# Performance work log

Measured on AMD Instinct MI355X. Metric: run time of the kernel, lower is better.

Reference implementation:

```python
import jax, jax.numpy as jnp
import numpy as np

N = 50000   # num_nodes
T = 8       # num_time_steps
C = 64      # feature width (num_features == hidden == num_classes == 64, forced by the module's shape constraints)
E = 800000  # num_edges


def temporal_conv(x, edge_index, time_index, W, b, perturb=None):
    """Faithful TemporalAGNNConv.forward: per-timestep masked scatter-add of
    neighbor features, concat over T, linear + relu. Implemented as a single
    fused (t, dst)-bucketed segment reduce instead of T separate propagates.
    Note: self.lin is dead code in the original; self-loop addition in the
    original would crash (time_index length mismatch) so edges are used as-is.
    """
    src, dst = edge_index[0], edge_index[1]
    msgs = x[src]                                   # [E, C] gather
    seg = time_index * N + dst                      # combined (t, node) bucket
    agg = jax.ops.segment_sum(msgs, seg, num_segments=T * N)   # [T*N, C]
    cat = agg.reshape(T, N, C).transpose(1, 0, 2).reshape(N, T * C)  # [N, T*C]
    out = jax.nn.relu(cat @ W + b)                  # temporal_lin + relu
    if perturb is not None:
        out = out + perturb
    return out


def setup_inputs() -> dict:
    key = jax.random.key(0)
    ks = jax.random.split(key, 11)
    x = jax.random.normal(ks[0], (N, C), jnp.float32)
    edge_index = jax.random.randint(ks[1], (2, E), 0, N, dtype=jnp.int32)
    time_index = jax.random.randint(ks[2], (E,), 0, T, dtype=jnp.int32)
    s_t = 1.0 / np.sqrt(T * C).astype(np.float32)
    # temporal_lin weights stored as [in, out] (torch Linear transposed)
    Wt1 = jax.random.uniform(ks[3], (T * C, C), jnp.float32, -s_t, s_t)
    bt1 = jax.random.uniform(ks[4], (C,), jnp.float32, -s_t, s_t)
    Wt2 = jax.random.uniform(ks[5], (T * C, C), jnp.float32, -s_t, s_t)
    bt2 = jax.random.uniform(ks[6], (C,), jnp.float32, -s_t, s_t)
    s_a1 = 1.0 / np.sqrt(C).astype(np.float32)
    Wa1 = jax.random.uniform(ks[7], (C, 128), jnp.float32, -s_a1, s_a1)
    ba1 = jax.random.uniform(ks[8], (128,), jnp.float32, -s_a1, s_a1)
    s_a2 = 1.0 / np.sqrt(128).astype(np.float32)
    Wa2 = jax.random.uniform(ks[9], (128, C), jnp.float32, -s_a2, s_a2)
    ba2 = jax.random.uniform(ks[10], (C,), jnp.float32, -s_a2, s_a2)
    return {"x": x, "edge_index": edge_index, "time_index": time_index,
            "Wt1": Wt1, "bt1": bt1, "Wt2": Wt2, "bt2": bt2,
            "Wa1": Wa1, "ba1": ba1, "Wa2": Wa2, "ba2": ba2}


def reference(x, edge_index, time_index, Wt1, bt1, Wt2, bt2, Wa1, ba1, Wa2, ba2):
    h1 = jax.nn.relu(temporal_conv(x, edge_index, time_index, Wt1, bt1))   # conv1 + relu
    h2 = temporal_conv(h1, edge_index, time_index, Wt2, bt2)               # conv2 (output width C)
    adv = jax.nn.relu(h2 @ Wa1 + ba1) @ Wa2 + ba2                          # adversary MLP -> [N, C]
    out = temporal_conv(x, edge_index, time_index, Wt1, bt1, perturb=adv)  # conv1 again + perturbation
    return out
```

## Files before the change

### kernel.cpp

```cpp
#include <hip/hip_runtime.h>

#define N_NODES 50000
#define C_FEAT  64
#define E_EDGES 800000
#define KEYS    400000
#define NBLK1   391
#define DPB     16
#define NTILES  (N_NODES / DPB)
#define PBLK_X  1563
#define PBLK_W  128
#define PBLK_A  64
#define PBLK_H  391
#define DPART   6250
#define CONV_GRID 1024

typedef __attribute__((ext_vector_type(8))) short short8;
typedef __attribute__((ext_vector_type(4))) float f32x4;

__device__ __forceinline__ float bf2f(unsigned short u) {
    union { unsigned int i; float f; } v; v.i = ((unsigned int)u) << 16; return v.f;
}
__device__ __forceinline__ unsigned short f2bf(float f) {
    union { float f; unsigned int i; } v; v.f = f;
    unsigned int r = v.i + 0x7fff + ((v.i >> 16) & 1);
    return (unsigned short)(r >> 16);
}

__global__ __launch_bounds__(256) void prep_hist(const float* __restrict__ x,
                                                 const float* __restrict__ W1,
                                                 const float* __restrict__ W2,
                                                 const float* __restrict__ Wa1,
                                                 const float* __restrict__ Wa2,
                                                 const int* __restrict__ dst,
                                                 const int* __restrict__ tix,
                                                 unsigned short* __restrict__ xb,
                                                 unsigned short* __restrict__ WT1,
                                                 unsigned short* __restrict__ WT2,
                                                 unsigned short* __restrict__ Wa1T,
                                                 unsigned short* __restrict__ Wa2T,
                                                 int* __restrict__ cnt) {
    const int b = blockIdx.x;
    if (b < PBLK_X) {
        int base = (b * 256 + threadIdx.x) * 8;
        if (base < N_NODES * 64) {
            float4 a = *(const float4*)(x + base);
            float4 c = *(const float4*)(x + base + 4);
            short8 o;
            o[0] = (short)f2bf(a.x); o[1] = (short)f2bf(a.y);
            o[2] = (short)f2bf(a.z); o[3] = (short)f2bf(a.w);
            o[4] = (short)f2bf(c.x); o[5] = (short)f2bf(c.y);
            o[6] = (short)f2bf(c.z); o[7] = (short)f2bf(c.w);
            *(short8*)(xb + base) = o;
        }
    } else if (b < PBLK_X + PBLK_W) {
        int i = (b - PBLK_X) * 256 + threadIdx.x;
        int n = i >> 9, k = i & 511;
        WT1[i] = f2bf(W1[k * 64 + n]);
        WT2[i] = f2bf(W2[k * 64 + n]);
    } else if (b < PBLK_X + PBLK_W + PBLK_A) {
        int i = (b - PBLK_X - PBLK_W) * 256 + threadIdx.x;
        if (i < 8192) {
            int n = i >> 6, k = i & 63;
            Wa1T[i] = f2bf(Wa1[k * 128 + n]);
        } else {
            int ii = i - 8192;
            int n = ii >> 7, k = ii & 127;
            Wa2T[ii] = f2bf(Wa2[k * 64 + n]);
        }
    } else {
        int bb = b - PBLK_X - PBLK_W - PBLK_A;
        const int e0 = bb * 2048 + threadIdx.x * 8;
        if (e0 < E_EDGES) {
            int4 d0 = *(const int4*)(dst + e0);
            int4 d1 = *(const int4*)(dst + e0 + 4);
            int4 t0 = *(const int4*)(tix + e0);
            int4 t1 = *(const int4*)(tix + e0 + 4);
            int dd[8] = {d0.x, d0.y, d0.z, d0.w, d1.x, d1.y, d1.z, d1.w};
            int tt[8] = {t0.x, t0.y, t0.z, t0.w, t1.x, t1.y, t1.z, t1.w};
            #pragma unroll
            for (int k = 0; k < 8; ++k)
                atomicAdd(&cnt[dd[k] * 8 + tt[k]], 1);
        }
    }
}

__global__ __launch_bounds__(256) void scan_all(int* __restrict__ cnt,
                                                int* __restrict__ bsum,
                                                int* __restrict__ chunkoff,
                                                int* __restrict__ done) {
    __shared__ int wsum[4];
    __shared__ int ticket;
    const int tid = threadIdx.x;
    const int lane = tid & 63;
    const int wave = tid >> 6;
    const int i4 = blockIdx.x * 256 + tid;
    int4 v = make_int4(0, 0, 0, 0);
    const bool ok = (i4 * 4 < KEYS);
    if (ok) v = ((const int4*)cnt)[i4];
    int s = v.x + v.y + v.z + v.w;
    int sc = s;
    #pragma unroll
    for (int d = 1; d < 64; d <<= 1) {
        int o = __shfl_up(sc, d, 64);
        if (lane >= d) sc += o;
    }
    if (lane == 63) wsum[wave] = sc;
    __syncthreads();
    int wbase = 0;
    #pragma unroll
    for (int w = 0; w < 4; ++w) wbase += (w < wave) ? wsum[w] : 0;
    int base = wbase + sc - s;
    int4 o;
    o.x = base;
    o.y = base + v.x;
    o.z = o.y + v.y;
    o.w = o.z + v.z;
    if (ok) ((int4*)cnt)[i4] = o;
    if (tid == 255) {
        bsum[blockIdx.x] = wbase + sc;
        __threadfence();
        ticket = atomicAdd(done, 1);
    }
    __syncthreads();
    if (ticket == NBLK1 - 1 && wave == 0) {
        int carry = 0;
        #pragma unroll
        for (int g = 0; g < (NBLK1 + 63) / 64; ++g) {
            int j = g * 64 + lane;
            int val = (j < NBLK1) ? atomicAdd(&bsum[j], 0) : 0;
            int scn = val;
            #pragma unroll
            for (int d = 1; d < 64; d <<= 1) {
                int oo = __shfl_up(scn, d, 64);
                if (lane >= d) scn += oo;
            }
            if (j < NBLK1) chunkoff[j] = carry + scn - val;
            carry += __shfl(scn, 63, 64);
        }
    }
}

__global__ __launch_bounds__(256) void scatter_edges(const int* __restrict__ src,
                                                     const int* __restrict__ dst,
                                                     const int* __restrict__ tix,
                                                     int* __restrict__ cursor,
                                                     const int* __restrict__ chunkoff,
                                                     int* __restrict__ elist) {
    const int g = blockIdx.x & 7;
    const int lo = g * DPART;
    const int e0 = (blockIdx.x >> 3) * 2048 + threadIdx.x * 8;
    if (e0 < E_EDGES) {
        int4 d0 = *(const int4*)(dst + e0);
        int4 d1 = *(const int4*)(dst + e0 + 4);
        int4 t0 = *(const int4*)(tix + e0);
        int4 t1 = *(const int4*)(tix + e0 + 4);
        int4 s0 = *(const int4*)(src + e0);
        int4 s1 = *(const int4*)(src + e0 + 4);
        int dd[8] = {d0.x, d0.y, d0.z, d0.w, d1.x, d1.y, d1.z, d1.w};
        int tt[8] = {t0.x, t0.y, t0.z, t0.w, t1.x, t1.y, t1.z, t1.w};
        int ss[8] = {s0.x, s0.y, s0.z, s0.w, s1.x, s1.y, s1.z, s1.w};
        #pragma unroll
        for (int k = 0; k < 8; ++k) {
            if ((unsigned)(dd[k] - lo) < (unsigned)DPART) {
                int key = dd[k] * 8 + tt[k];
                int pos = chunkoff[key >> 10] + atomicAdd(&cursor[key], 1);
                elist[pos] = ss[k] | (tt[k] << 16);
            }
        }
    }
}

#define FLUSH(T, V)                                                                   \
    { int _t = (T);                                                                   \
      if (_t != cur) { scat[dl][cur * 64 + c] = f2bf(acc); acc = 0.f; cur = _t; }     \
      acc += (V); }

#define EDGE(K)                                                                       \
    int p##K = __builtin_amdgcn_readlane(pv, e + K);                                  \
    float v##K = bf2f(Xb[(size_t)(p##K & 0xffff) * 64 + c]);

__global__ __launch_bounds__(512, 8) void fused_conv(const unsigned short* __restrict__ Xb,
                                                     const unsigned short* __restrict__ WT,
                                                     const float* __restrict__ bias,
                                                     const int* __restrict__ segend,
                                                     const int* __restrict__ chunkoff,
                                                     const int* __restrict__ elist,
                                                     unsigned short* __restrict__ Hb) {
    __shared__ unsigned short scat[DPB][520];
    const int lane = threadIdx.x & 63;
    const int wave = threadIdx.x >> 6;
    const int c = lane;

    for (int tile = blockIdx.x; tile < NTILES; tile += gridDim.x) {
        const int dbase = tile * DPB;

        {
            short8 z = {};
            *(short8*)&scat[wave * 2 + 0][lane * 8] = z;
            *(short8*)&scat[wave * 2 + 1][lane * 8] = z;
        }

        int sbeg[2], send_[2], pvw[2];
        #pragma unroll
        for (int q = 0; q < 2; ++q) {
            const int d = dbase + wave * 2 + q;
            const int k0 = d * 8;
            sbeg[q]  = (d == 0) ? 0 : chunkoff[(k0 - 1) >> 10] + segend[k0 - 1];
            send_[q] = chunkoff[(k0 + 7) >> 10] + segend[k0 + 7];
        }
        #pragma unroll
        for (int q = 0; q < 2; ++q)
            pvw[q] = (lane < send_[q] - sbeg[q]) ? elist[sbeg[q] + lane] : 0;

        #pragma unroll
        for (int q = 0; q < 2; ++q) {
            const int dl = wave * 2 + q;
            int i = sbeg[q];
            const int end = send_[q];
            int pv = pvw[q];
            int cur = 0;
            float acc = 0.f;
            while (i < end) {
                int cnt = end - i; cnt = (cnt > 64) ? 64 : cnt;
                int pvn = 0;
                if (i + 64 < end) pvn = (lane < end - i - 64) ? elist[i + 64 + lane] : 0;
                int e = 0;
                for (; e + 15 < cnt; e += 16) {
                    EDGE(0)  EDGE(1)  EDGE(2)  EDGE(3)
                    EDGE(4)  EDGE(5)  EDGE(6)  EDGE(7)
                    EDGE(8)  EDGE(9)  EDGE(10) EDGE(11)
                    EDGE(12) EDGE(13) EDGE(14) EDGE(15)
                    FLUSH(p0 >> 16, v0)   FLUSH(p1 >> 16, v1)
                    FLUSH(p2 >> 16, v2)   FLUSH(p3 >> 16, v3)
                    FLUSH(p4 >> 16, v4)   FLUSH(p5 >> 16, v5)
                    FLUSH(p6 >> 16, v6)   FLUSH(p7 >> 16, v7)
                    FLUSH(p8 >> 16, v8)   FLUSH(p9 >> 16, v9)
                    FLUSH(p10 >> 16, v10) FLUSH(p11 >> 16, v11)
                    FLUSH(p12 >> 16, v12) FLUSH(p13 >> 16, v13)
                    FLUSH(p14 >> 16, v14) FLUSH(p15 >> 16, v15)
                }
                if (e + 7 < cnt) {
                    EDGE(0) EDGE(1) EDGE(2) EDGE(3) EDGE(4) EDGE(5) EDGE(6) EDGE(7)
                    FLUSH(p0 >> 16, v0) FLUSH(p1 >> 16, v1)
                    FLUSH(p2 >> 16, v2) FLUSH(p3 >> 16, v3)
                    FLUSH(p4 >> 16, v4) FLUSH(p5 >> 16, v5)
                    FLUSH(p6 >> 16, v6) FLUSH(p7 >> 16, v7)
                    e += 8;
                }
                if (e + 3 < cnt) {
                    EDGE(0) EDGE(1) EDGE(2) EDGE(3)
                    FLUSH(p0 >> 16, v0) FLUSH(p1 >> 16, v1)
                    FLUSH(p2 >> 16, v2) FLUSH(p3 >> 16, v3)
                    e += 4;
                }
                if (e + 1 < cnt) {
                    EDGE(0) EDGE(1)
                    FLUSH(p0 >> 16, v0) FLUSH(p1 >> 16, v1)
                    e += 2;
                }
                if (e < cnt) {
                    EDGE(0)
                    FLUSH(p0 >> 16, v0)
                }
                i += 64;
                pv = pvn;
            }
            scat[dl][cur * 64 + c] = f2bf(acc);
        }
        __syncthreads();

        if (wave < 4) {
            const int m = lane & 15;
            const int quad = lane >> 4;
            const int n0 = wave * 16;
            f32x4 acc4 = {0.f, 0.f, 0.f, 0.f};
            const unsigned short* wrow = WT + (size_t)(n0 + m) * 512;
            #pragma unroll
            for (int kc = 0; kc < 16; ++kc) {
                short8 af = *(const short8*)&scat[m][kc * 32 + quad * 8];
                short8 bf = *(const short8*)(wrow + kc * 32 + quad * 8);
                acc4 = __builtin_amdgcn_mfma_f32_16x16x32_bf16(af, bf, acc4, 0, 0, 0);
            }
            const int col = n0 + m;
            const float bcol = bias[col];
            #pragma unroll
            for (int r = 0; r < 4; ++r) {
                int node = dbase + quad * 4 + r;
                Hb[(size_t)node * 64 + col] = f2bf(fmaxf(acc4[r] + bcol, 0.f));
            }
        }
        __syncthreads();
    }
}

__global__ __launch_bounds__(256) void adv_mfma(const unsigned short* __restrict__ h2b,
                                                const unsigned short* __restrict__ Wa1T,
                                                const float* __restrict__ ba1,
                                                const unsigned short* __restrict__ Wa2T,
                                                const float* __restrict__ ba2,
                                                const unsigned short* __restrict__ h1b,
                                                float* __restrict__ out) {
    __shared__ unsigned short sH[64][72];
    __shared__ unsigned short sT[64][136];
    const int nbase = blockIdx.x * 64;
    const int tid = threadIdx.x;
    const int lane = tid & 63;
    const int wave = tid >> 6;
    const int m = lane & 15;
    const int quad = lane >> 4;
    const int r0 = wave * 16;

    #pragma unroll
    for (int i = 0; i < 2; ++i) {
        int idx = tid * 2 + i;
        int row = idx >> 3;
        int c8  = (idx & 7) * 8;
        int node = nbase + row;
        short8 u = {};
        if (node < N_NODES)
            u = *(const short8*)(h2b + (size_t)node * C_FEAT + c8);
        *(short8*)&sH[row][c8] = u;
    }
    __syncthreads();

    {
        f32x4 acc1[8];
        #pragma unroll
        for (int ct = 0; ct < 8; ++ct) acc1[ct] = (f32x4){0.f, 0.f, 0.f, 0.f};
        #pragma unroll
        for (int kc = 0; kc < 2; ++kc) {
            short8 af = *(const short8*)&sH[r0 + m][kc * 32 + quad * 8];
            #pragma unroll
            for (int ct = 0; ct < 8; ++ct) {
                short8 bf = *(const short8*)(Wa1T + (size_t)(ct * 16 + m) * 64 + kc * 32 + quad * 8);
                acc1[ct] = __builtin_amdgcn_mfma_f32_16x16x32_bf16(af, bf, acc1[ct], 0, 0, 0);
            }
        }
        #pragma unroll
        for (int ct = 0; ct < 8; ++ct) {
            const int col = ct * 16 + m;
            const float b1 = ba1[col];
            #pragma unroll
            for (int r = 0; r < 4; ++r)
                sT[r0 + quad * 4 + r][col] = f2bf(fmaxf(acc1[ct][r] + b1, 0.f));
        }
    }
    __syncthreads();

    {
        f32x4 acc2[4];
        #pragma unroll
        for (int ct = 0; ct < 4; ++ct) acc2[ct] = (f32x4){0.f, 0.f, 0.f, 0.f};
        #pragma unroll
        for (int kc = 0; kc < 4; ++kc) {
            short8 af = *(const short8*)&sT[r0 + m][kc * 32 + quad * 8];
            #pragma unroll
            for (int ct = 0; ct < 4; ++ct) {
                short8 bf = *(const short8*)(Wa2T + (size_t)(ct * 16 + m) * 128 + kc * 32 + quad * 8);
                acc2[ct] = __builtin_amdgcn_mfma_f32_16x16x32_bf16(af, bf, acc2[ct], 0, 0, 0);
            }
        }
        #pragma unroll
        for (int ct = 0; ct < 4; ++ct) {
            const int col = ct * 16 + m;
            const float b2 = ba2[col];
            #pragma unroll
            for (int r = 0; r < 4; ++r) {
                int node = nbase + r0 + quad * 4 + r;
                if (node < N_NODES) {
                    float val = acc2[ct][r] + b2 + bf2f(h1b[(size_t)node * 64 + col]);
                    out[(size_t)node * 64 + col] = val;
                }
            }
        }
    }
}

extern "C" void kernel_launch(void* const* d_in, const int* in_sizes, int n_in,
                              void* d_out, int out_size, void* d_ws, size_t ws_size,
                              hipStream_t stream) {
    const float* x   = (const float*)d_in[0];
    const int*   ei  = (const int*)d_in[1];
    const int*   tix = (const int*)d_in[2];
    const float* Wt1 = (const float*)d_in[3];
    const float* bt1 = (const float*)d_in[4];
    const float* Wt2 = (const float*)d_in[5];
    const float* bt2 = (const float*)d_in[6];
    const float* Wa1 = (const float*)d_in[7];
    const float* ba1 = (const float*)d_in[8];
    const float* Wa2 = (const float*)d_in[9];
    const float* ba2 = (const float*)d_in[10];
    float* out = (float*)d_out;

    const int* src = ei;
    const int* dst = ei + E_EDGES;

    unsigned short* xb   = (unsigned short*)d_ws;
    unsigned short* h1b  = xb + (size_t)N_NODES * 64;
    unsigned short* h2b  = h1b + (size_t)N_NODES * 64;
    unsigned short* WT1  = h2b + (size_t)N_NODES * 64;
    unsigned short* WT2  = WT1 + 64 * 512;
    unsigned short* Wa1T = WT2 + 64 * 512;
    unsigned short* Wa2T = Wa1T + 8192;
    int* cnt      = (int*)(Wa2T + 8192);
    int* bsum     = cnt + KEYS;
    int* chunkoff = bsum + 512;
    int* done     = chunkoff + 512;
    int* elist    = done + 64;

    const int aBlk = (N_NODES + 63) / 64;

    hipMemsetAsync(cnt, 0, (KEYS + 512 + 512 + 64) * sizeof(int), stream);
    prep_hist<<<PBLK_X + PBLK_W + PBLK_A + PBLK_H, 256, 0, stream>>>(
        x, Wt1, Wt2, Wa1, Wa2, dst, tix, xb, WT1, WT2, Wa1T, Wa2T, cnt);
    scan_all<<<NBLK1, 256, 0, stream>>>(cnt, bsum, chunkoff, done);
    scatter_edges<<<8 * 391, 256, 0, stream>>>(src, dst, tix, cnt, chunkoff, elist);

    fused_conv<<<CONV_GRID, 512, 0, stream>>>(xb,  WT1, bt1, cnt, chunkoff, elist, h1b);
    fused_conv<<<CONV_GRID, 512, 0, stream>>>(h1b, WT2, bt2, cnt, chunkoff, elist, h2b);

    adv_mfma<<<aBlk, 256, 0, stream>>>(h2b, Wa1T, ba1, Wa2T, ba2, h1b, out);
}
```

Measured before the change: 289.8 us.

## Pre-bucket edges by destination partition and load-balance conv destinations dynamically

```diff
diff --git a/kernel.cpp b/kernel.cpp
--- a/kernel.cpp
+++ b/kernel.cpp
@@ -10,8 +10,9 @@
 #define PBLK_X  1563
 #define PBLK_W  128
 #define PBLK_A  64
-#define PBLK_H  391
+#define PBLK_P  391
 #define DPART   6250
+#define BUCKSZ  131072
 #define CONV_GRID 1024
 
 typedef __attribute__((ext_vector_type(8))) short short8;
@@ -31,6 +32,7 @@
                                                  const float* __restrict__ W2,
                                                  const float* __restrict__ Wa1,
                                                  const float* __restrict__ Wa2,
+                                                 const int* __restrict__ src,
                                                  const int* __restrict__ dst,
                                                  const int* __restrict__ tix,
                                                  unsigned short* __restrict__ xb,
@@ -38,7 +40,11 @@
                                                  unsigned short* __restrict__ WT2,
                                                  unsigned short* __restrict__ Wa1T,
                                                  unsigned short* __restrict__ Wa2T,
-                                                 int* __restrict__ cnt) {
+                                                 int* __restrict__ cnt,
+                                                 int* __restrict__ bcur,
+                                                 int2* __restrict__ staging) {
+    __shared__ int lcnt[8], lbase[8], lcur[8], gbase[8];
+    __shared__ int2 lrec[2048];
     const int b = blockIdx.x;
     if (b < PBLK_X) {
         int base = (b * 256 + threadIdx.x) * 8;
@@ -70,16 +76,55 @@
     } else {
         int bb = b - PBLK_X - PBLK_W - PBLK_A;
         const int e0 = bb * 2048 + threadIdx.x * 8;
-        if (e0 < E_EDGES) {
+        const bool valid = (e0 < E_EDGES);
+        if (threadIdx.x < 8) { lcnt[threadIdx.x] = 0; lcur[threadIdx.x] = 0; }
+        int dd[8], tt[8], ss[8];
+        if (valid) {
             int4 d0 = *(const int4*)(dst + e0);
             int4 d1 = *(const int4*)(dst + e0 + 4);
             int4 t0 = *(const int4*)(tix + e0);
             int4 t1 = *(const int4*)(tix + e0 + 4);
-            int dd[8] = {d0.x, d0.y, d0.z, d0.w, d1.x, d1.y, d1.z, d1.w};
-            int tt[8] = {t0.x, t0.y, t0.z, t0.w, t1.x, t1.y, t1.z, t1.w};
-            #pragma unroll
-            for (int k = 0; k < 8; ++k)
+            int4 s0 = *(const int4*)(src + e0);
+            int4 s1 = *(const int4*)(src + e0 + 4);
+            dd[0]=d0.x; dd[1]=d0.y; dd[2]=d0.z; dd[3]=d0.w;
+            dd[4]=d1.x; dd[5]=d1.y; dd[6]=d1.z; dd[7]=d1.w;
+            tt[0]=t0.x; tt[1]=t0.y; tt[2]=t0.z; tt[3]=t0.w;
+            tt[4]=t1.x; tt[5]=t1.y; tt[6]=t1.z; tt[7]=t1.w;
+            ss[0]=s0.x; ss[1]=s0.y; ss[2]=s0.z; ss[3]=s0.w;
+            ss[4]=s1.x; ss[5]=s1.y; ss[6]=s1.z; ss[7]=s1.w;
+        }
+        __syncthreads();
+        if (valid) {
+            #pragma unroll
+            for (int k = 0; k < 8; ++k) {
                 atomicAdd(&cnt[dd[k] * 8 + tt[k]], 1);
+                atomicAdd(&lcnt[dd[k] / DPART], 1);
+            }
+        }
+        __syncthreads();
+        if (threadIdx.x == 0) {
+            int run = 0;
+            #pragma unroll
+            for (int g = 0; g < 8; ++g) { lbase[g] = run; run += lcnt[g]; }
+        }
+        __syncthreads();
+        if (valid) {
+            #pragma unroll
+            for (int k = 0; k < 8; ++k) {
+                int g = dd[k] / DPART;
+                int p = lbase[g] + atomicAdd(&lcur[g], 1);
+                lrec[p] = make_int2(ss[k] | (tt[k] << 16), dd[k] * 8 + tt[k]);
+            }
+        }
+        __syncthreads();
+        if (threadIdx.x < 8)
+            gbase[threadIdx.x] = atomicAdd(&bcur[threadIdx.x], lcnt[threadIdx.x]);
+        __syncthreads();
+        #pragma unroll
+        for (int g = 0; g < 8; ++g) {
+            const int n = lcnt[g], lb = lbase[g], gb = gbase[g];
+            for (int i = threadIdx.x; i < n; i += 256)
+                staging[(size_t)g * BUCKSZ + gb + i] = lrec[lb + i];
         }
     }
 }
@@ -140,33 +185,34 @@
     }
 }
 
-__global__ __launch_bounds__(256) void scatter_edges(const int* __restrict__ src,
-                                                     const int* __restrict__ dst,
-                                                     const int* __restrict__ tix,
+__global__ __launch_bounds__(256) void scatter_edges(const int2* __restrict__ staging,
+                                                     const int* __restrict__ bcur,
                                                      int* __restrict__ cursor,
                                                      const int* __restrict__ chunkoff,
                                                      int* __restrict__ elist) {
     const int g = blockIdx.x & 7;
-    const int lo = g * DPART;
-    const int e0 = (blockIdx.x >> 3) * 2048 + threadIdx.x * 8;
-    if (e0 < E_EDGES) {
-        int4 d0 = *(const int4*)(dst + e0);
-        int4 d1 = *(const int4*)(dst + e0 + 4);
-        int4 t0 = *(const int4*)(tix + e0);
-        int4 t1 = *(const int4*)(tix + e0 + 4);
-        int4 s0 = *(const int4*)(src + e0);
-        int4 s1 = *(const int4*)(src + e0 + 4);
-        int dd[8] = {d0.x, d0.y, d0.z, d0.w, d1.x, d1.y, d1.z, d1.w};
-        int tt[8] = {t0.x, t0.y, t0.z, t0.w, t1.x, t1.y, t1.z, t1.w};
-        int ss[8] = {s0.x, s0.y, s0.z, s0.w, s1.x, s1.y, s1.z, s1.w};
-        #pragma unroll
-        for (int k = 0; k < 8; ++k) {
-            if ((unsigned)(dd[k] - lo) < (unsigned)DPART) {
-                int key = dd[k] * 8 + tt[k];
-                int pos = chunkoff[key >> 10] + atomicAdd(&cursor[key], 1);
-                elist[pos] = ss[k] | (tt[k] << 16);
-            }
-        }
+    const int j = blockIdx.x >> 3;
+    const int nrec = bcur[g];
+    const int r0 = j * 1024 + threadIdx.x * 4;
+    if (r0 >= nrec) return;
+    const int2* base = staging + (size_t)g * BUCKSZ;
+    int4 a = *(const int4*)(base + r0);
+    int4 b = *(const int4*)(base + r0 + 2);
+    {
+        int pos = chunkoff[a.y >> 10] + atomicAdd(&cursor[a.y], 1);
+        elist[pos] = a.x;
+    }
+    if (r0 + 1 < nrec) {
+        int pos = chunkoff[a.w >> 10] + atomicAdd(&cursor[a.w], 1);
+        elist[pos] = a.z;
+    }
+    if (r0 + 2 < nrec) {
+        int pos = chunkoff[b.y >> 10] + atomicAdd(&cursor[b.y], 1);
+        elist[pos] = b.x;
+    }
+    if (r0 + 3 < nrec) {
+        int pos = chunkoff[b.w >> 10] + atomicAdd(&cursor[b.w], 1);
+        elist[pos] = b.z;
     }
 }
 
@@ -187,11 +233,12 @@
                                                      const int* __restrict__ elist,
                                                      unsigned short* __restrict__ Hb) {
     __shared__ unsigned short scat[DPB][520];
+    __shared__ int nextd;
     const int lane = threadIdx.x & 63;
     const int wave = threadIdx.x >> 6;
     const int c = lane;
 
-    for (int tile = blockIdx.x; tile < NTILES; tile += gridDim.x) {
+    for (int tile = blockIdx.x; tile < NTILES; tile += CONV_GRID) {
         const int dbase = tile * DPB;
 
         {
@@ -199,31 +246,39 @@
             *(short8*)&scat[wave * 2 + 0][lane * 8] = z;
             *(short8*)&scat[wave * 2 + 1][lane * 8] = z;
         }
-
-        int sbeg[2], send_[2], pvw[2];
-        #pragma unroll
-        for (int q = 0; q < 2; ++q) {
-            const int d = dbase + wave * 2 + q;
-            const int k0 = d * 8;
-            sbeg[q]  = (d == 0) ? 0 : chunkoff[(k0 - 1) >> 10] + segend[k0 - 1];
-            send_[q] = chunkoff[(k0 + 7) >> 10] + segend[k0 + 7];
-        }
-        #pragma unroll
-        for (int q = 0; q < 2; ++q)
-            pvw[q] = (lane < send_[q] - sbeg[q]) ? elist[sbeg[q] + lane] : 0;
-
-        #pragma unroll
-        for (int q = 0; q < 2; ++q) {
-            const int dl = wave * 2 + q;
-            int i = sbeg[q];
-            const int end = send_[q];
-            int pv = pvw[q];
+        if (threadIdx.x == 0) nextd = 0;
+        __syncthreads();
+
+        int q_ = 0;
+        if (lane == 0) q_ = atomicAdd(&nextd, 1);
+        int qn = __shfl(q_, 0, 64);
+        int sbn = 0, sen = 0, pvn = 0;
+        if (qn < DPB) {
+            const int d = dbase + qn, k0 = d * 8;
+            sbn = (d == 0) ? 0 : chunkoff[(k0 - 1) >> 10] + segend[k0 - 1];
+            sen = chunkoff[(k0 + 7) >> 10] + segend[k0 + 7];
+            pvn = (lane < sen - sbn) ? elist[sbn + lane] : 0;
+        }
+        while (qn < DPB) {
+            const int dl = qn;
+            int i = sbn;
+            const int end = sen;
+            int pv = pvn;
+            int t_ = 0;
+            if (lane == 0) t_ = atomicAdd(&nextd, 1);
+            qn = __shfl(t_, 0, 64);
+            if (qn < DPB) {
+                const int d = dbase + qn, k0 = d * 8;
+                sbn = (d == 0) ? 0 : chunkoff[(k0 - 1) >> 10] + segend[k0 - 1];
+                sen = chunkoff[(k0 + 7) >> 10] + segend[k0 + 7];
+                pvn = (lane < sen - sbn) ? elist[sbn + lane] : 0;
+            }
             int cur = 0;
             float acc = 0.f;
             while (i < end) {
                 int cnt = end - i; cnt = (cnt > 64) ? 64 : cnt;
-                int pvn = 0;
-                if (i + 64 < end) pvn = (lane < end - i - 64) ? elist[i + 64 + lane] : 0;
+                int pv2 = 0;
+                if (i + 64 < end) pv2 = (lane < end - i - 64) ? elist[i + 64 + lane] : 0;
                 int e = 0;
                 for (; e + 15 < cnt; e += 16) {
                     EDGE(0)  EDGE(1)  EDGE(2)  EDGE(3)
@@ -263,7 +318,7 @@
                     FLUSH(p0 >> 16, v0)
                 }
                 i += 64;
-                pv = pvn;
+                pv = pv2;
             }
             scat[dl][cur * 64 + c] = f2bf(acc);
         }
@@ -406,15 +461,18 @@
     int* bsum     = cnt + KEYS;
     int* chunkoff = bsum + 512;
     int* done     = chunkoff + 512;
-    int* elist    = done + 64;
+    int* bcur     = done + 64;
+    int* elist    = bcur + 64;
+    int2* staging = (int2*)(elist + E_EDGES);
 
     const int aBlk = (N_NODES + 63) / 64;
 
-    hipMemsetAsync(cnt, 0, (KEYS + 512 + 512 + 64) * sizeof(int), stream);
-    prep_hist<<<PBLK_X + PBLK_W + PBLK_A + PBLK_H, 256, 0, stream>>>(
-        x, Wt1, Wt2, Wa1, Wa2, dst, tix, xb, WT1, WT2, Wa1T, Wa2T, cnt);
+    hipMemsetAsync(cnt, 0, (KEYS + 512 + 512 + 64 + 64) * sizeof(int), stream);
+    prep_hist<<<PBLK_X + PBLK_W + PBLK_A + PBLK_P, 256, 0, stream>>>(
+        x, Wt1, Wt2, Wa1, Wa2, src, dst, tix, xb, WT1, WT2, Wa1T, Wa2T,
+        cnt, bcur, staging);
     scan_all<<<NBLK1, 256, 0, stream>>>(cnt, bsum, chunkoff, done);
-    scatter_edges<<<8 * 391, 256, 0, stream>>>(src, dst, tix, cnt, chunkoff, elist);
+    scatter_edges<<<1024, 256, 0, stream>>>(staging, bcur, cnt, chunkoff, elist);
 
     fused_conv<<<CONV_GRID, 512, 0, stream>>>(xb,  WT1, bt1, cnt, chunkoff, elist, h1b);
     fused_conv<<<CONV_GRID, 512, 0, stream>>>(h1b, WT2, bt2, cnt, chunkoff, elist, h2b);
```

Measured after the change: 296.9 us. 1.02x slower.

## Fuse adversary MLP into second conv and merge two-node edge walks per wave

Applied to the files above, without the earlier changes.

```diff
diff --git a/kernel.cpp b/kernel.cpp
--- a/kernel.cpp
+++ b/kernel.cpp
@@ -164,34 +164,44 @@
             if ((unsigned)(dd[k] - lo) < (unsigned)DPART) {
                 int key = dd[k] * 8 + tt[k];
                 int pos = chunkoff[key >> 10] + atomicAdd(&cursor[key], 1);
-                elist[pos] = ss[k] | (tt[k] << 16);
-            }
-        }
-    }
-}
-
-#define FLUSH(T, V)                                                                   \
-    { int _t = (T);                                                                   \
-      if (_t != cur) { scat[dl][cur * 64 + c] = f2bf(acc); acc = 0.f; cur = _t; }     \
+                elist[pos] = ss[k] | (tt[k] << 16) | ((dd[k] & 15) << 19);
+            }
+        }
+    }
+}
+
+#define FLUSH(P, V)                                                                   \
+    { int _k = (P) >> 16;                                                             \
+      if (_k != cur) { scat[cur >> 3][(cur & 7) * 64 + c] = f2bf(acc);                \
+                       acc = 0.f; cur = _k; }                                         \
       acc += (V); }
 
 #define EDGE(K)                                                                       \
     int p##K = __builtin_amdgcn_readlane(pv, e + K);                                  \
     float v##K = bf2f(Xb[(size_t)(p##K & 0xffff) * 64 + c]);
 
+template <bool ADV>
 __global__ __launch_bounds__(512, 8) void fused_conv(const unsigned short* __restrict__ Xb,
                                                      const unsigned short* __restrict__ WT,
                                                      const float* __restrict__ bias,
                                                      const int* __restrict__ segend,
                                                      const int* __restrict__ chunkoff,
                                                      const int* __restrict__ elist,
-                                                     unsigned short* __restrict__ Hb) {
-    __shared__ unsigned short scat[DPB][520];
+                                                     unsigned short* __restrict__ Hb,
+                                                     const unsigned short* __restrict__ Wa1T,
+                                                     const float* __restrict__ ba1,
+                                                     const unsigned short* __restrict__ Wa2T,
+                                                     const float* __restrict__ ba2,
+                                                     const unsigned short* __restrict__ h1r,
+                                                     float* __restrict__ outF) {
+    __shared__ __attribute__((aligned(16))) unsigned short scat[DPB][520];
+    unsigned short (*sH)[72]  = (unsigned short(*)[72])&scat[0][0];
+    unsigned short (*sT)[136] = (unsigned short(*)[136])((char*)scat + 4096);
     const int lane = threadIdx.x & 63;
     const int wave = threadIdx.x >> 6;
     const int c = lane;
 
-    for (int tile = blockIdx.x; tile < NTILES; tile += gridDim.x) {
+    for (int tile = blockIdx.x; tile < NTILES; tile += CONV_GRID) {
         const int dbase = tile * DPB;
 
         {
@@ -200,80 +210,84 @@
             *(short8*)&scat[wave * 2 + 1][lane * 8] = z;
         }
 
-        int sbeg[2], send_[2], pvw[2];
-        #pragma unroll
-        for (int q = 0; q < 2; ++q) {
-            const int d = dbase + wave * 2 + q;
-            const int k0 = d * 8;
-            sbeg[q]  = (d == 0) ? 0 : chunkoff[(k0 - 1) >> 10] + segend[k0 - 1];
-            send_[q] = chunkoff[(k0 + 7) >> 10] + segend[k0 + 7];
-        }
-        #pragma unroll
-        for (int q = 0; q < 2; ++q)
-            pvw[q] = (lane < send_[q] - sbeg[q]) ? elist[sbeg[q] + lane] : 0;
-
-        #pragma unroll
-        for (int q = 0; q < 2; ++q) {
-            const int dl = wave * 2 + q;
-            int i = sbeg[q];
-            const int end = send_[q];
-            int pv = pvw[q];
+        const int dpair = dbase + wave * 2;
+        const int k0 = dpair * 8;
+        const int sbeg = (dpair == 0) ? 0 : chunkoff[(k0 - 1) >> 10] + segend[k0 - 1];
+        const int send = chunkoff[(k0 + 15) >> 10] + segend[k0 + 15];
+        int pv = (lane < send - sbeg) ? elist[sbeg + lane] : 0;
+
+        {
+            int i = sbeg;
             int cur = 0;
             float acc = 0.f;
-            while (i < end) {
-                int cnt = end - i; cnt = (cnt > 64) ? 64 : cnt;
+            if (i < send) cur = __builtin_amdgcn_readlane(pv, 0) >> 16;
+            while (i < send) {
+                int cnt = send - i; cnt = (cnt > 64) ? 64 : cnt;
                 int pvn = 0;
-                if (i + 64 < end) pvn = (lane < end - i - 64) ? elist[i + 64 + lane] : 0;
+                if (i + 64 < send) pvn = (lane < send - i - 64) ? elist[i + 64 + lane] : 0;
                 int e = 0;
-                for (; e + 15 < cnt; e += 16) {
+                for (; e + 31 < cnt; e += 32) {
                     EDGE(0)  EDGE(1)  EDGE(2)  EDGE(3)
                     EDGE(4)  EDGE(5)  EDGE(6)  EDGE(7)
                     EDGE(8)  EDGE(9)  EDGE(10) EDGE(11)
                     EDGE(12) EDGE(13) EDGE(14) EDGE(15)
-                    FLUSH(p0 >> 16, v0)   FLUSH(p1 >> 16, v1)
-                    FLUSH(p2 >> 16, v2)   FLUSH(p3 >> 16, v3)
-                    FLUSH(p4 >> 16, v4)   FLUSH(p5 >> 16, v5)
-                    FLUSH(p6 >> 16, v6)   FLUSH(p7 >> 16, v7)
-                    FLUSH(p8 >> 16, v8)   FLUSH(p9 >> 16, v9)
-                    FLUSH(p10 >> 16, v10) FLUSH(p11 >> 16, v11)
-                    FLUSH(p12 >> 16, v12) FLUSH(p13 >> 16, v13)
-                    FLUSH(p14 >> 16, v14) FLUSH(p15 >> 16, v15)
+                    EDGE(16) EDGE(17) EDGE(18) EDGE(19)
+                    EDGE(20) EDGE(21) EDGE(22) EDGE(23)
+                    EDGE(24) EDGE(25) EDGE(26) EDGE(27)
+                    EDGE(28) EDGE(29) EDGE(30) EDGE(31)
+                    FLUSH(p0, v0)   FLUSH(p1, v1)   FLUSH(p2, v2)   FLUSH(p3, v3)
+                    FLUSH(p4, v4)   FLUSH(p5, v5)   FLUSH(p6, v6)   FLUSH(p7, v7)
+                    FLUSH(p8, v8)   FLUSH(p9, v9)   FLUSH(p10, v10) FLUSH(p11, v11)
+                    FLUSH(p12, v12) FLUSH(p13, v13) FLUSH(p14, v14) FLUSH(p15, v15)
+                    FLUSH(p16, v16) FLUSH(p17, v17) FLUSH(p18, v18) FLUSH(p19, v19)
+                    FLUSH(p20, v20) FLUSH(p21, v21) FLUSH(p22, v22) FLUSH(p23, v23)
+                    FLUSH(p24, v24) FLUSH(p25, v25) FLUSH(p26, v26) FLUSH(p27, v27)
+                    FLUSH(p28, v28) FLUSH(p29, v29) FLUSH(p30, v30) FLUSH(p31, v31)
+                }
+                if (e + 15 < cnt) {
+                    EDGE(0)  EDGE(1)  EDGE(2)  EDGE(3)
+                    EDGE(4)  EDGE(5)  EDGE(6)  EDGE(7)
+                    EDGE(8)  EDGE(9)  EDGE(10) EDGE(11)
+                    EDGE(12) EDGE(13) EDGE(14) EDGE(15)
+                    FLUSH(p0, v0)   FLUSH(p1, v1)   FLUSH(p2, v2)   FLUSH(p3, v3)
+                    FLUSH(p4, v4)   FLUSH(p5, v5)   FLUSH(p6, v6)   FLUSH(p7, v7)
+                    FLUSH(p8, v8)   FLUSH(p9, v9)   FLUSH(p10, v10) FLUSH(p11, v11)
+                    FLUSH(p12, v12) FLUSH(p13, v13) FLUSH(p14, v14) FLUSH(p15, v15)
+                    e += 16;
                 }
                 if (e + 7 < cnt) {
                     EDGE(0) EDGE(1) EDGE(2) EDGE(3) EDGE(4) EDGE(5) EDGE(6) EDGE(7)
-                    FLUSH(p0 >> 16, v0) FLUSH(p1 >> 16, v1)
-                    FLUSH(p2 >> 16, v2) FLUSH(p3 >> 16, v3)
-                    FLUSH(p4 >> 16, v4) FLUSH(p5 >> 16, v5)
-                    FLUSH(p6 >> 16, v6) FLUSH(p7 >> 16, v7)
+                    FLUSH(p0, v0) FLUSH(p1, v1) FLUSH(p2, v2) FLUSH(p3, v3)
+                    FLUSH(p4, v4) FLUSH(p5, v5) FLUSH(p6, v6) FLUSH(p7, v7)
                     e += 8;
                 }
                 if (e + 3 < cnt) {
                     EDGE(0) EDGE(1) EDGE(2) EDGE(3)
-                    FLUSH(p0 >> 16, v0) FLUSH(p1 >> 16, v1)
-                    FLUSH(p2 >> 16, v2) FLUSH(p3 >> 16, v3)
+                    FLUSH(p0, v0) FLUSH(p1, v1) FLUSH(p2, v2) FLUSH(p3, v3)
                     e += 4;
                 }
                 if (e + 1 < cnt) {
                     EDGE(0) EDGE(1)
-                    FLUSH(p0 >> 16, v0) FLUSH(p1 >> 16, v1)
+                    FLUSH(p0, v0) FLUSH(p1, v1)
                     e += 2;
                 }
                 if (e < cnt) {
                     EDGE(0)
-                    FLUSH(p0 >> 16, v0)
+                    FLUSH(p0, v0)
                 }
                 i += 64;
                 pv = pvn;
             }
-            scat[dl][cur * 64 + c] = f2bf(acc);
+            if (sbeg < send)
+                scat[cur >> 3][(cur & 7) * 64 + c] = f2bf(acc);
         }
         __syncthreads();
 
+        const int m = lane & 15;
+        const int quad = lane >> 4;
+        f32x4 acc4 = {0.f, 0.f, 0.f, 0.f};
         if (wave < 4) {
-            const int m = lane & 15;
-            const int quad = lane >> 4;
             const int n0 = wave * 16;
-            f32x4 acc4 = {0.f, 0.f, 0.f, 0.f};
             const unsigned short* wrow = WT + (size_t)(n0 + m) * 512;
             #pragma unroll
             for (int kc = 0; kc < 16; ++kc) {
@@ -281,98 +295,62 @@
                 short8 bf = *(const short8*)(wrow + kc * 32 + quad * 8);
                 acc4 = __builtin_amdgcn_mfma_f32_16x16x32_bf16(af, bf, acc4, 0, 0, 0);
             }
-            const int col = n0 + m;
-            const float bcol = bias[col];
-            #pragma unroll
-            for (int r = 0; r < 4; ++r) {
-                int node = dbase + quad * 4 + r;
-                Hb[(size_t)node * 64 + col] = f2bf(fmaxf(acc4[r] + bcol, 0.f));
+        }
+
+        if (!ADV) {
+            if (wave < 4) {
+                const int col = wave * 16 + m;
+                const float bcol = bias[col];
+                #pragma unroll
+                for (int r = 0; r < 4; ++r) {
+                    int node = dbase + quad * 4 + r;
+                    Hb[(size_t)node * 64 + col] = f2bf(fmaxf(acc4[r] + bcol, 0.f));
+                }
+            }
+        } else {
+            __syncthreads();
+            if (wave < 4) {
+                const int col = wave * 16 + m;
+                const float bcol = bias[col];
+                #pragma unroll
+                for (int r = 0; r < 4; ++r)
+                    sH[quad * 4 + r][col] = f2bf(fmaxf(acc4[r] + bcol, 0.f));
+            }
+            __syncthreads();
+            {
+                f32x4 a1 = {0.f, 0.f, 0.f, 0.f};
+                const int col = wave * 16 + m;
+                #pragma unroll
+                for (int kc = 0; kc < 2; ++kc) {
+                    short8 af = *(const short8*)&sH[m][kc * 32 + quad * 8];
+                    short8 bf = *(const short8*)(Wa1T + (size_t)col * 64 + kc * 32 + quad * 8);
+                    a1 = __builtin_amdgcn_mfma_f32_16x16x32_bf16(af, bf, a1, 0, 0, 0);
+                }
+                const float b1 = ba1[col];
+                #pragma unroll
+                for (int r = 0; r < 4; ++r)
+                    sT[quad * 4 + r][col] = f2bf(fmaxf(a1[r] + b1, 0.f));
+            }
+            __syncthreads();
+            if (wave < 4) {
+                f32x4 a2 = {0.f, 0.f, 0.f, 0.f};
+                const int col = wave * 16 + m;
+                #pragma unroll
+                for (int kc = 0; kc < 4; ++kc) {
+                    short8 af = *(const short8*)&sT[m][kc * 32 + quad * 8];
+                    short8 bf = *(const short8*)(Wa2T + (size_t)col * 128 + kc * 32 + quad * 8);
+                    a2 = __builtin_amdgcn_mfma_f32_16x16x32_bf16(af, bf, a2, 0, 0, 0);
+                }
+                const float b2 = ba2[col];
+                #pragma unroll
+                for (int r = 0; r < 4; ++r) {
+                    int node = dbase + quad * 4 + r;
+                    outF[(size_t)node * 64 + col] =
+                        a2[r] + b2 + bf2f(h1r[(size_t)node * 64 + col]);
+                }
             }
         }
         __syncthreads();
-    }
-}
-
-__global__ __launch_bounds__(256) void adv_mfma(const unsigned short* __restrict__ h2b,
-                                                const unsigned short* __restrict__ Wa1T,
-                                                const float* __restrict__ ba1,
-                                                const unsigned short* __restrict__ Wa2T,
-                                                const float* __restrict__ ba2,
-                                                const unsigned short* __restrict__ h1b,
-                                                float* __restrict__ out) {
-    __shared__ unsigned short sH[64][72];
-    __shared__ unsigned short sT[64][136];
-    const int nbase = blockIdx.x * 64;
-    const int tid = threadIdx.x;
-    const int lane = tid & 63;
-    const int wave = tid >> 6;
-    const int m = lane & 15;
-    const int quad = lane >> 4;
-    const int r0 = wave * 16;
-
-    #pragma unroll
-    for (int i = 0; i < 2; ++i) {
-        int idx = tid * 2 + i;
-        int row = idx >> 3;
-        int c8  = (idx & 7) * 8;
-        int node = nbase + row;
-        short8 u = {};
-        if (node < N_NODES)
-            u = *(const short8*)(h2b + (size_t)node * C_FEAT + c8);
-        *(short8*)&sH[row][c8] = u;
-    }
-    __syncthreads();
-
-    {
-        f32x4 acc1[8];
-        #pragma unroll
-        for (int ct = 0; ct < 8; ++ct) acc1[ct] = (f32x4){0.f, 0.f, 0.f, 0.f};
-        #pragma unroll
-        for (int kc = 0; kc < 2; ++kc) {
-            short8 af = *(const short8*)&sH[r0 + m][kc * 32 + quad * 8];
-            #pragma unroll
-            for (int ct = 0; ct < 8; ++ct) {
-                short8 bf = *(const short8*)(Wa1T + (size_t)(ct * 16 + m) * 64 + kc * 32 + quad * 8);
-                acc1[ct] = __builtin_amdgcn_mfma_f32_16x16x32_bf16(af, bf, acc1[ct], 0, 0, 0);
-            }
-        }
-        #pragma unroll
-        for (int ct = 0; ct < 8; ++ct) {
-            const int col = ct * 16 + m;
-            const float b1 = ba1[col];
-            #pragma unroll
-            for (int r = 0; r < 4; ++r)
-                sT[r0 + quad * 4 + r][col] = f2bf(fmaxf(acc1[ct][r] + b1, 0.f));
-        }
-    }
-    __syncthreads();
-
-    {
-        f32x4 acc2[4];
-        #pragma unroll
-        for (int ct = 0; ct < 4; ++ct) acc2[ct] = (f32x4){0.f, 0.f, 0.f, 0.f};
-        #pragma unroll
-        for (int kc = 0; kc < 4; ++kc) {
-            short8 af = *(const short8*)&sT[r0 + m][kc * 32 + quad * 8];
-            #pragma unroll
-            for (int ct = 0; ct < 4; ++ct) {
-                short8 bf = *(const short8*)(Wa2T + (size_t)(ct * 16 + m) * 128 + kc * 32 + quad * 8);
-                acc2[ct] = __builtin_amdgcn_mfma_f32_16x16x32_bf16(af, bf, acc2[ct], 0, 0, 0);
-            }
-        }
-        #pragma unroll
-        for (int ct = 0; ct < 4; ++ct) {
-            const int col = ct * 16 + m;
-            const float b2 = ba2[col];
-            #pragma unroll
-            for (int r = 0; r < 4; ++r) {
-                int node = nbase + r0 + quad * 4 + r;
-                if (node < N_NODES) {
-                    float val = acc2[ct][r] + b2 + bf2f(h1b[(size_t)node * 64 + col]);
-                    out[(size_t)node * 64 + col] = val;
-                }
-            }
-        }
     }
 }
 
@@ -408,16 +386,16 @@
     int* done     = chunkoff + 512;
     int* elist    = done + 64;
 
-    const int aBlk = (N_NODES + 63) / 64;
-
     hipMemsetAsync(cnt, 0, (KEYS + 512 + 512 + 64) * sizeof(int), stream);
     prep_hist<<<PBLK_X + PBLK_W + PBLK_A + PBLK_H, 256, 0, stream>>>(
         x, Wt1, Wt2, Wa1, Wa2, dst, tix, xb, WT1, WT2, Wa1T, Wa2T, cnt);
     scan_all<<<NBLK1, 256, 0, stream>>>(cnt, bsum, chunkoff, done);
     scatter_edges<<<8 * 391, 256, 0, stream>>>(src, dst, tix, cnt, chunkoff, elist);
 
-    fused_conv<<<CONV_GRID, 512, 0, stream>>>(xb,  WT1, bt1, cnt, chunkoff, elist, h1b);
-    fused_conv<<<CONV_GRID, 512, 0, stream>>>(h1b, WT2, bt2, cnt, chunkoff, elist, h2b);
-
-    adv_mfma<<<aBlk, 256, 0, stream>>>(h2b, Wa1T, ba1, Wa2T, ba2, h1b, out);
-}
+    fused_conv<false><<<CONV_GRID, 512, 0, stream>>>(
+        xb, WT1, bt1, cnt, chunkoff, elist, h1b,
+        nullptr, nullptr, nullptr, nullptr, nullptr, nullptr);
+    fused_conv<true><<<CONV_GRID, 512, 0, stream>>>(
+        h1b, WT2, bt2, cnt, chunkoff, elist, nullptr,
+        Wa1T, ba1, Wa2T, ba2, h1b, out);
+}
```

After: 281.8 us. -2.8%, faster.
